# Kernel optimization log

Hardware: AMD Instinct MI355X
Metric: run time of the kernel (lower is better)

## Reference

```python
import jax, jax.numpy as jnp
import numpy as np

N_FFT = 4096
HOP = 1024
WIN = 4096
DIAG_EPS = 1e-7
EPS = 1e-8

# asteroid-style periodic sqrt-hann analysis/synthesis window
_n = np.arange(WIN)
WINDOW = jnp.asarray(np.sqrt(0.5 - 0.5 * np.cos(2.0 * np.pi * _n / WIN)), dtype=jnp.float32)


def _frame_idx(n_samp):
    T = (n_samp - WIN) // HOP + 1
    return np.arange(T)[:, None] * HOP + np.arange(WIN)[None, :]


def stft(x):
    """x: (..., N) -> (real, imag) each (..., F, T) with F = N_FFT//2+1."""
    idx = _frame_idx(x.shape[-1])
    frames = x[..., idx] * WINDOW
    spec = jnp.fft.rfft(frames, axis=-1)     # (..., T, F) complex64
    spec = jnp.moveaxis(spec, -2, -1)        # (..., F, T)
    return spec.real, spec.imag


def istft(re, im, out_len):
    """(..., F, T) -> (..., out_len) via windowed overlap-add."""
    spec = jnp.moveaxis(re + 1j * im, -1, -2)            # (..., T, F)
    frames = jnp.fft.irfft(spec, n=WIN, axis=-1) * WINDOW
    T = frames.shape[-2]
    full = (T - 1) * HOP + WIN
    idx = _frame_idx(full).reshape(-1)
    flat = frames.reshape(frames.shape[:-2] + (-1,))
    out = jnp.zeros(frames.shape[:-2] + (full,), frames.dtype).at[..., idx].add(flat)
    wsq = jnp.zeros((full,), jnp.float32).at[idx].add(jnp.tile(WINDOW ** 2, T))
    out = out / jnp.maximum(wsq, 1e-8)
    return out[..., :out_len]


def psd_causal(re, im):
    """Causal, frame-normalized PSD. re/im: (B, C, F, T) -> complex (B, T, F, C, C)."""
    pr = jnp.einsum('saft,sbft->sabft', re, re) + jnp.einsum('saft,sbft->sabft', im, im)
    pi = jnp.einsum('saft,sbft->sbaft', re, im) - jnp.einsum('saft,sbft->sabft', re, im)
    cnt = jnp.arange(1, re.shape[-1] + 1, dtype=re.dtype)
    pr = jnp.cumsum(pr, -1) / cnt
    pi = jnp.cumsum(pi, -1) / cnt
    psd = pr + 1j * pi                       # (B, a, b, F, T)
    return jnp.transpose(psd, (0, 4, 3, 1, 2))  # (B, T, F, C, C)


def mvdr_vector(psd_s, psd_n):
    """Souden MVDR: ws = inv(Npsd) @ Spsd / (tr(.) + eps). (..., C, C) complex."""
    C = psd_n.shape[-1]
    tr_n = jnp.trace(psd_n, axis1=-2, axis2=-1).real
    epsilon = jax.lax.stop_gradient(tr_n * DIAG_EPS + EPS)
    psd_n = psd_n + epsilon[..., None, None] * jnp.eye(C, dtype=psd_n.dtype)
    num = jnp.linalg.inv(psd_n) @ psd_s
    return num / (jnp.trace(num, axis1=-2, axis2=-1)[..., None, None] + EPS)


def _forward(x, s):
    B, S, C, N = s.shape
    xs = jnp.broadcast_to(x[:, None], (B, S, C, N)).reshape(B * S, C, N)
    ss = s.reshape(B * S, C, N)
    Xr, Xi = stft(xs)
    Sr, Si = stft(ss)
    Nr, Ni = Xr - Sr, Xi - Si
    Sscm = psd_causal(Sr, Si)   # (BS, T, F, C, C)
    Nscm = psd_causal(Nr, Ni)
    ws = mvdr_vector(Sscm, Nscm)  # (BS, T, F, C, C)
    # conj(filter), rearranged to (BS, a, b, F, T)
    fr = jnp.transpose(ws.real, (0, 3, 4, 2, 1))
    fi = -jnp.transpose(ws.imag, (0, 3, 4, 2, 1))
    enh_r = jnp.einsum('sabft,saft->sbft', fr, Xr) - jnp.einsum('sabft,saft->sbft', fi, Xi)
    enh_i = jnp.einsum('sabft,saft->sbft', fr, Xi) + jnp.einsum('sabft,saft->sbft', fi, Xr)
    est = istft(enh_r, enh_i, N)            # (BS, C, N)
    return est.reshape(B, S, C, N)


def setup_inputs() -> dict:
    key = jax.random.key(0)
    kx, ks = jax.random.split(key)
    x = jax.random.normal(kx, (2, 4, 32768), dtype=jnp.float32)
    s = jax.random.normal(ks, (2, 2, 4, 32768), dtype=jnp.float32)
    return {"x": x, "s": s, "do_permute": 0}


def reference(x, s, do_permute):
    # do_permute=False path (PIT permutation is a data-dependent preprocessing step)
    return _forward(x, s)
```

## Files before the change

### kernel.cpp

```cpp
#include <hip/hip_runtime.h>

static constexpr int NFFT = 4096;
static constexpr int HOP  = 1024;
static constexpr int NF   = 2049;
static constexpr int NT   = 29;
static constexpr int NS   = 32768;
static constexpr int NB   = 2;
static constexpr int NSrc = 2;
static constexpr int NC   = 4;
static constexpr int NBS  = NB * NSrc;
static constexpr int FCHUNKS = (NF + 7) / 8;

#define PI_F     3.14159265358979323846f
#define TWO_PI_F 6.28318530717958647692f

#define IDX(a) ((a) + ((a) >> 4))
static constexpr int LDSN = 2048 + 128;

__device__ inline float2 cmul(float2 a, float2 b) {
    return make_float2(a.x * b.x - a.y * b.y, a.x * b.y + a.y * b.x);
}
__device__ inline float2 cmulc(float2 a, float2 b) {
    return make_float2(a.x * b.x + a.y * b.y, a.y * b.x - a.x * b.y);
}

template <int CTRL, int RMASK>
__device__ __forceinline__ float dpp0(float x) {
    return __int_as_float(__builtin_amdgcn_update_dpp(
        0, __float_as_int(x), CTRL, RMASK, 0xF, true));
}

template <int DIR>
__device__ inline void fft4v(float2 v[4]) {
    float2 t0 = make_float2(v[0].x + v[2].x, v[0].y + v[2].y);
    float2 t1 = make_float2(v[0].x - v[2].x, v[0].y - v[2].y);
    float2 t2 = make_float2(v[1].x + v[3].x, v[1].y + v[3].y);
    float2 t3 = make_float2(v[1].x - v[3].x, v[1].y - v[3].y);
    v[0] = make_float2(t0.x + t2.x, t0.y + t2.y);
    v[2] = make_float2(t0.x - t2.x, t0.y - t2.y);
    if (DIR < 0) {
        v[1] = make_float2(t1.x + t3.y, t1.y - t3.x);
        v[3] = make_float2(t1.x - t3.y, t1.y + t3.x);
    } else {
        v[1] = make_float2(t1.x - t3.y, t1.y + t3.x);
        v[3] = make_float2(t1.x + t3.y, t1.y - t3.x);
    }
}

template <int DIR>
__device__ inline void fft8v(float2 v[8]) {
    float2 e[4] = { v[0], v[2], v[4], v[6] };
    float2 o[4] = { v[1], v[3], v[5], v[7] };
    fft4v<DIR>(e);
    fft4v<DIR>(o);
    const float c = 0.70710678118654752f;
    float2 o0 = o[0], o1, o2, o3;
    if (DIR < 0) {
        o1 = make_float2(c * (o[1].x + o[1].y), c * (o[1].y - o[1].x));
        o2 = make_float2(o[2].y, -o[2].x);
        o3 = make_float2(c * (o[3].y - o[3].x), -c * (o[3].x + o[3].y));
    } else {
        o1 = make_float2(c * (o[1].x - o[1].y), c * (o[1].y + o[1].x));
        o2 = make_float2(-o[2].y, o[2].x);
        o3 = make_float2(-c * (o[3].x + o[3].y), c * (o[3].x - o[3].y));
    }
    v[0] = make_float2(e[0].x + o0.x, e[0].y + o0.y);
    v[4] = make_float2(e[0].x - o0.x, e[0].y - o0.y);
    v[1] = make_float2(e[1].x + o1.x, e[1].y + o1.y);
    v[5] = make_float2(e[1].x - o1.x, e[1].y - o1.y);
    v[2] = make_float2(e[2].x + o2.x, e[2].y + o2.y);
    v[6] = make_float2(e[2].x - o2.x, e[2].y - o2.y);
    v[3] = make_float2(e[3].x + o3.x, e[3].y + o3.y);
    v[7] = make_float2(e[3].x - o3.x, e[3].y - o3.y);
}

template <int DIR, int NSs>
__device__ inline void stage8(const float* __restrict__ reS, const float* __restrict__ imS,
                              float* __restrict__ reD, float* __restrict__ imD, int tid) {
    int j = tid;
    float2 v[8];
    #pragma unroll
    for (int r = 0; r < 8; ++r) {
        int a = IDX(j + (r << 8));
        v[r] = make_float2(reS[a], imS[a]);
    }
    if (NSs > 1) {
        float ang = (float)DIR * (TWO_PI_F / (8.0f * (float)NSs)) * (float)(j & (NSs - 1));
        float2 w1; __sincosf(ang, &w1.y, &w1.x);
        float2 w2 = cmul(w1, w1);
        float2 w3 = cmul(w2, w1);
        float2 w4 = cmul(w2, w2);
        float2 w5 = cmul(w3, w2);
        float2 w6 = cmul(w3, w3);
        float2 w7 = cmul(w4, w3);
        v[1] = cmul(v[1], w1);
        v[2] = cmul(v[2], w2);
        v[3] = cmul(v[3], w3);
        v[4] = cmul(v[4], w4);
        v[5] = cmul(v[5], w5);
        v[6] = cmul(v[6], w6);
        v[7] = cmul(v[7], w7);
    }
    fft8v<DIR>(v);
    int idxD = ((j & ~(NSs - 1)) << 3) + (j & (NSs - 1));
    #pragma unroll
    for (int r = 0; r < 8; ++r) {
        int a = IDX(idxD + r * NSs);
        reD[a] = v[r].x;
        imD[a] = v[r].y;
    }
}

template <int DIR>
__device__ inline void stage4_512(const float* __restrict__ reS, const float* __restrict__ imS,
                                  float* __restrict__ reD, float* __restrict__ imD, int tid) {
    #pragma unroll
    for (int h = 0; h < 2; ++h) {
        int j = tid + (h << 8);
        float2 v[4];
        #pragma unroll
        for (int r = 0; r < 4; ++r) {
            int a = IDX(j + (r << 9));
            v[r] = make_float2(reS[a], imS[a]);
        }
        float ang = (float)DIR * (TWO_PI_F / 2048.0f) * (float)j;
        float2 w1; __sincosf(ang, &w1.y, &w1.x);
        float2 w2 = cmul(w1, w1);
        float2 w3 = cmul(w2, w1);
        v[1] = cmul(v[1], w1);
        v[2] = cmul(v[2], w2);
        v[3] = cmul(v[3], w3);
        fft4v<DIR>(v);
        #pragma unroll
        for (int r = 0; r < 4; ++r) {
            int a = IDX(j + (r << 9));
            reD[a] = v[r].x;
            imD[a] = v[r].y;
        }
    }
}

template <int DIR>
__device__ inline void fft2048(float* reA, float* imA, float* reB, float* imB, int tid) {
    stage8<DIR, 1>(reA, imA, reB, imB, tid);  __syncthreads();
    stage8<DIR, 8>(reB, imB, reA, imA, tid);  __syncthreads();
    stage8<DIR, 64>(reA, imA, reB, imB, tid); __syncthreads();
    stage4_512<DIR>(reB, imB, reA, imA, tid); __syncthreads();
}

__global__ __launch_bounds__(256) void stft_kernel(
    const float* __restrict__ x, const float* __restrict__ s,
    float2* __restrict__ Xs, float2* __restrict__ Ss) {
    __shared__ float reA[LDSN], imA[LDSN], reB[LDSN], imB[LDSN];
    int tid = threadIdx.x;
    int fid = blockIdx.x;
    const float* src;
    float2* dst;
    if (fid < NB * NC * NT) {
        int b = fid / (NC * NT);
        int r = fid % (NC * NT);
        int c = r / NT;
        int t = r % NT;
        src = x + (size_t)((b * NC + c) * NS + t * HOP);
        dst = Xs + (size_t)((b * NC + c) * NT + t) * NF;
    } else {
        int g  = fid - NB * NC * NT;
        int bs = g / (NC * NT);
        int r  = g % (NC * NT);
        int c  = r / NT;
        int t  = r % NT;
        src = s + (size_t)((bs * NC + c) * NS + t * HOP);
        dst = Ss + (size_t)((bs * NC + c) * NT + t) * NF;
    }
    const float2* s2 = (const float2*)src;
    for (int n = tid; n < 2048; n += 256) {
        float2 v = s2[n];
        float we = __sinf((float)n * (PI_F / 2048.0f));
        float wo = __sinf((float)(2 * n + 1) * (PI_F / 4096.0f));
        int a = IDX(n);
        reA[a] = v.x * we;
        imA[a] = v.y * wo;
    }
    __syncthreads();
    fft2048<-1>(reA, imA, reB, imB, tid);
    for (int k = tid; k <= 1024; k += 256) {
        int a1 = IDX(k);
        int a2 = IDX((2048 - k) & 2047);
        float2 Za = make_float2(reA[a1], imA[a1]);
        float2 Zb = make_float2(reA[a2], imA[a2]);
        if (k == 0) {
            dst[0]    = make_float2(Za.x + Za.y, 0.f);
            dst[2048] = make_float2(Za.x - Za.y, 0.f);
        } else {
            float2 Ze = make_float2(0.5f * (Za.x + Zb.x),  0.5f * (Za.y - Zb.y));
            float2 Zo = make_float2(0.5f * (Za.y + Zb.y), -0.5f * (Za.x - Zb.x));
            float ang = -(PI_F / 2048.0f) * (float)k;
            float2 W; __sincosf(ang, &W.y, &W.x);
            float2 WZo = cmul(W, Zo);
            dst[k] = make_float2(Ze.x + WZo.x, Ze.y + WZo.y);
            if (k < 1024)
                dst[2048 - k] = make_float2(Ze.x - WZo.x, -(Ze.y - WZo.y));
        }
    }
}

__global__ __launch_bounds__(256, 1) void mvdr2_kernel(
    const float2* __restrict__ Xs, const float2* __restrict__ Ss,
    float2* __restrict__ Es) {
    __shared__ float2 ldsS[4][32][9];
    __shared__ float2 ldsX[4][32][9];
    int tid = threadIdx.x;
    int blk = blockIdx.x;
    int bs  = blk / FCHUNKS;
    int f0  = (blk % FCHUNKS) * 8;
    int b   = bs >> 1;

    for (int idx = tid; idx < 2048; idx += 256) {
        int fi = idx & 7;
        int tt = (idx >> 3) & 31;
        int q  = idx >> 8;
        int c  = q & 3;
        int f  = f0 + fi;
        float2 val = make_float2(0.f, 0.f);
        if (tt < NT && f < NF) {
            val = (q >= 4) ? Xs[(size_t)((b  * NC + c) * NT + tt) * NF + f]
                           : Ss[(size_t)((bs * NC + c) * NT + tt) * NF + f];
        }
        if (q >= 4) ldsX[c][tt][fi] = val; else ldsS[c][tt][fi] = val;
    }
    __syncthreads();

    int lane  = tid & 63;
    int wave  = tid >> 6;
    int t     = lane & 31;
    int fpair = lane >> 5;
    int fi    = wave * 2 + fpair;

    float2 Sv[4], Xv[4], Nv[4];
    #pragma unroll
    for (int c = 0; c < 4; ++c) {
        Sv[c] = ldsS[c][t][fi];
        Xv[c] = ldsX[c][t][fi];
        Nv[c] = make_float2(Xv[c].x - Sv[c].x, Xv[c].y - Sv[c].y);
    }

    float v[32];
    #pragma unroll
    for (int c = 0; c < 4; ++c) {
        v[c]      = Sv[c].x * Sv[c].x + Sv[c].y * Sv[c].y;
        v[16 + c] = Nv[c].x * Nv[c].x + Nv[c].y * Nv[c].y;
    }
    constexpr int PI6[6] = {0, 0, 0, 1, 1, 2};
    constexpr int PJ6[6] = {1, 2, 3, 2, 3, 3};
    #pragma unroll
    for (int p = 0; p < 6; ++p) {
        float2 d = cmulc(Sv[PI6[p]], Sv[PJ6[p]]);
        v[4 + 2 * p] = d.x; v[5 + 2 * p] = d.y;
        d = cmulc(Nv[PI6[p]], Nv[PJ6[p]]);
        v[20 + 2 * p] = d.x; v[21 + 2 * p] = d.y;
    }

    #pragma unroll
    for (int k = 0; k < 32; ++k) v[k] += dpp0<0x111, 0xF>(v[k]);
    #pragma unroll
    for (int k = 0; k < 32; ++k) v[k] += dpp0<0x112, 0xF>(v[k]);
    #pragma unroll
    for (int k = 0; k < 32; ++k) v[k] += dpp0<0x114, 0xF>(v[k]);
    #pragma unroll
    for (int k = 0; k < 32; ++k) v[k] += dpp0<0x118, 0xF>(v[k]);
    #pragma unroll
    for (int k = 0; k < 32; ++k) v[k] += dpp0<0x142, 0xA>(v[k]);

    float pd0 = v[0], pd1 = v[1], pd2 = v[2], pd3 = v[3];
    float2 po0 = make_float2(v[4],  v[5]);
    float2 po1 = make_float2(v[6],  v[7]);
    float2 po2 = make_float2(v[8],  v[9]);
    float2 po3 = make_float2(v[10], v[11]);
    float2 po4 = make_float2(v[12], v[13]);
    float2 po5 = make_float2(v[14], v[15]);
    float eps = (v[16] + v[17] + v[18] + v[19]) * 1e-7f + (float)(t + 1) * 1e-8f;
    float nd0 = v[16] + eps, nd1 = v[17] + eps, nd2 = v[18] + eps, nd3 = v[19] + eps;
    float2 no0 = make_float2(v[20], v[21]);
    float2 no1 = make_float2(v[22], v[23]);
    float2 no2 = make_float2(v[24], v[25]);
    float2 no3 = make_float2(v[26], v[27]);
    float2 no4 = make_float2(v[28], v[29]);
    float2 no5 = make_float2(v[30], v[31]);

    float D0 = nd0;
    float r0 = __builtin_amdgcn_rcpf(D0);
    float2 L10 = make_float2(no0.x * r0, -no0.y * r0);
    float2 L20 = make_float2(no1.x * r0, -no1.y * r0);
    float2 L30 = make_float2(no2.x * r0, -no2.y * r0);
    float D1 = nd1 - (L10.x * L10.x + L10.y * L10.y) * D0;
    float r1 = __builtin_amdgcn_rcpf(D1);
    float2 c10 = make_float2(D0 * L10.x, -D0 * L10.y);
    float2 tA = cmul(L20, c10);
    float2 L21 = make_float2((no3.x - tA.x) * r1, (-no3.y - tA.y) * r1);
    float2 tB = cmul(L30, c10);
    float2 L31 = make_float2((no4.x - tB.x) * r1, (-no4.y - tB.y) * r1);
    float D2 = nd2 - (L20.x * L20.x + L20.y * L20.y) * D0
                   - (L21.x * L21.x + L21.y * L21.y) * D1;
    float r2 = __builtin_amdgcn_rcpf(D2);
    float2 c20 = make_float2(D0 * L20.x, -D0 * L20.y);
    float2 c21 = make_float2(D1 * L21.x, -D1 * L21.y);
    float2 tC = cmul(L30, c20);
    float2 tD = cmul(L31, c21);
    float2 L32 = make_float2((no5.x - tC.x - tD.x) * r2, (-no5.y - tC.y - tD.y) * r2);
    float D3 = nd3 - (L30.x * L30.x + L30.y * L30.y) * D0
                   - (L31.x * L31.x + L31.y * L31.y) * D1
                   - (L32.x * L32.x + L32.y * L32.y) * D2;
    float r3 = __builtin_amdgcn_rcpf(D3);

    float2 u0 = Xv[0];
    float2 m0 = cmul(L10, u0);
    float2 u1 = make_float2(Xv[1].x - m0.x, Xv[1].y - m0.y);
    float2 m1 = cmul(L20, u0), m2 = cmul(L21, u1);
    float2 u2 = make_float2(Xv[2].x - m1.x - m2.x, Xv[2].y - m1.y - m2.y);
    float2 m3 = cmul(L30, u0), m4 = cmul(L31, u1), m5 = cmul(L32, u2);
    float2 u3 = make_float2(Xv[3].x - m3.x - m4.x - m5.x,
                            Xv[3].y - m3.y - m4.y - m5.y);
    float2 w0 = make_float2(u0.x * r0, u0.y * r0);
    float2 w1 = make_float2(u1.x * r1, u1.y * r1);
    float2 w2 = make_float2(u2.x * r2, u2.y * r2);
    float2 w3 = make_float2(u3.x * r3, u3.y * r3);
    float2 z3 = w3;
    float2 n0_ = cmulc(z3, L32);
    float2 z2 = make_float2(w2.x - n0_.x, w2.y - n0_.y);
    float2 n1_ = cmulc(z2, L21), n2_ = cmulc(z3, L31);
    float2 z1 = make_float2(w1.x - n1_.x - n2_.x, w1.y - n1_.y - n2_.y);
    float2 n3_ = cmulc(z1, L10), n4_ = cmulc(z2, L20), n5_ = cmulc(z3, L30);
    float2 z0 = make_float2(w0.x - n3_.x - n4_.x - n5_.x,
                            w0.y - n3_.y - n4_.y - n5_.y);

    float2 K10 = make_float2(-L10.x, -L10.y);
    float2 kk  = cmul(L21, L10);
    float2 K20 = make_float2(kk.x - L20.x, kk.y - L20.y);
    float2 K21 = make_float2(-L21.x, -L21.y);
    kk = cmul(L32, L21);
    float2 K31 = make_float2(kk.x - L31.x, kk.y - L31.y);
    float2 K32 = make_float2(-L32.x, -L32.y);
    float2 ka = cmul(K31, L10), kb = cmul(L32, L20);
    float2 K30 = make_float2(-L30.x - ka.x + kb.x, -L30.y - ka.y + kb.y);

    float q0 = pd0;
    float2 qm = cmul(K10, po0);
    float q1 = pd1 + (K10.x * K10.x + K10.y * K10.y) * pd0 + 2.0f * qm.x;
    qm = cmul(K20, po0);
    float s_a = qm.x * K21.x + qm.y * K21.y;
    qm = cmul(K20, po1);
    float s_b = qm.x;
    qm = cmul(K21, po3);
    float s_c = qm.x;
    float q2 = pd2 + (K20.x * K20.x + K20.y * K20.y) * pd0
                   + (K21.x * K21.x + K21.y * K21.y) * pd1
                   + 2.0f * (s_a + s_b + s_c);
    qm = cmul(K30, po0);
    float s1 = qm.x * K31.x + qm.y * K31.y;
    qm = cmul(K30, po1);
    float s2 = qm.x * K32.x + qm.y * K32.y;
    qm = cmul(K30, po2);
    float s3 = qm.x;
    qm = cmul(K31, po3);
    float s4 = qm.x * K32.x + qm.y * K32.y;
    qm = cmul(K31, po4);
    float s5 = qm.x;
    qm = cmul(K32, po5);
    float s6 = qm.x;
    float q3 = pd3 + (K30.x * K30.x + K30.y * K30.y) * pd0
                   + (K31.x * K31.x + K31.y * K31.y) * pd1
                   + (K32.x * K32.x + K32.y * K32.y) * pd2
                   + 2.0f * (s1 + s2 + s3 + s4 + s5 + s6);
    float tr = q0 * r0 + q1 * r1 + q2 * r2 + q3 * r3;
    float g  = __builtin_amdgcn_rcpf(tr + 1e-8f);

    float2 a0 = cmul(po0, z1), a1 = cmul(po1, z2), a2 = cmul(po2, z3);
    float2 e0 = make_float2(pd0 * z0.x + a0.x + a1.x + a2.x,
                            pd0 * z0.y + a0.y + a1.y + a2.y);
    a0 = cmulc(z0, po0); a1 = cmul(po3, z2); a2 = cmul(po4, z3);
    float2 e1 = make_float2(a0.x + pd1 * z1.x + a1.x + a2.x,
                            a0.y + pd1 * z1.y + a1.y + a2.y);
    a0 = cmulc(z0, po1); a1 = cmulc(z1, po3); a2 = cmul(po5, z3);
    float2 e2 = make_float2(a0.x + a1.x + pd2 * z2.x + a2.x,
                            a0.y + a1.y + pd2 * z2.y + a2.y);
    a0 = cmulc(z0, po2); a1 = cmulc(z1, po4); a2 = cmulc(z2, po5);
    float2 e3 = make_float2(a0.x + a1.x + a2.x + pd3 * z3.x,
                            a0.y + a1.y + a2.y + pd3 * z3.y);
    ldsS[0][t][fi] = make_float2(e0.x * g, e0.y * g);
    ldsS[1][t][fi] = make_float2(e1.x * g, e1.y * g);
    ldsS[2][t][fi] = make_float2(e2.x * g, e2.y * g);
    ldsS[3][t][fi] = make_float2(e3.x * g, e3.y * g);
    __syncthreads();

    for (int idx = tid; idx < 1024; idx += 256) {
        int fi2 = idx & 7;
        int tt  = (idx >> 3) & 31;
        int bo  = idx >> 8;
        int ff  = f0 + fi2;
        if (tt < NT && ff < NF)
            Es[(size_t)((bs * NC + bo) * NT + tt) * NF + ff] = ldsS[bo][tt][fi2];
    }
}

__global__ __launch_bounds__(256) void istft_kernel(
    const float2* __restrict__ Es, float* __restrict__ Fr) {
    __shared__ float reA[LDSN], imA[LDSN], reB[LDSN], imB[LDSN];
    int tid = threadIdx.x;
    int fid = blockIdx.x;
    int bs = fid / (NC * NT);
    int r  = fid % (NC * NT);
    int c  = r / NT;
    int t  = r % NT;
    const float2* src = Es + (size_t)((bs * NC + c) * NT + t) * NF;
    for (int k = tid; k <= 1024; k += 256) {
        float2 A = src[k];
        float2 B = src[2048 - k];
        float2 Ze = make_float2(0.5f * (A.x + B.x), 0.5f * (A.y - B.y));
        float2 D  = make_float2(0.5f * (A.x - B.x), 0.5f * (A.y + B.y));
        float ang = (PI_F / 2048.0f) * (float)k;
        float2 W; __sincosf(ang, &W.y, &W.x);
        float2 Zo = cmul(W, D);
        int a1 = IDX(k);
        reA[a1] = Ze.x - Zo.y;
        imA[a1] = Ze.y + Zo.x;
        if (k > 0 && k < 1024) {
            int a2 = IDX(2048 - k);
            reA[a2] = Ze.x + Zo.y;
            imA[a2] = -Ze.y + Zo.x;
        }
    }
    __syncthreads();
    fft2048<1>(reA, imA, reB, imB, tid);
    float2* d2 = (float2*)(Fr + (size_t)((bs * NC + c) * NT + t) * NFFT);
    for (int n = tid; n < 2048; n += 256) {
        int a = IDX(n);
        float we = __sinf((float)n * (PI_F / 2048.0f)) * (1.0f / 2048.0f);
        float wo = __sinf((float)(2 * n + 1) * (PI_F / 4096.0f)) * (1.0f / 2048.0f);
        d2[n] = make_float2(reA[a] * we, imA[a] * wo);
    }
}

__global__ __launch_bounds__(256) void ola_kernel(
    const float* __restrict__ Fr, float* __restrict__ out) {
    int idx = blockIdx.x * 256 + threadIdx.x;
    const int total = NBS * NC * NS;
    if (idx >= total) return;
    int p  = idx & (NS - 1);
    int ch = idx >> 15;
    int t1 = p >> 10;
    if (t1 > NT - 1) t1 = NT - 1;
    int t0 = (p >= NFFT) ? ((p - (NFFT - 1) + (HOP - 1)) >> 10) : 0;
    float acc = 0.f;
    for (int t = t0; t <= t1; ++t)
        acc += Fr[((size_t)(ch * NT + t) << 12) + (p - (t << 10))];
    float wacc;
    if (t1 - t0 == 3) {
        wacc = 2.0f;
    } else {
        wacc = 0.f;
        for (int t = t0; t <= t1; ++t) {
            float w = __sinf((float)(p - (t << 10)) * (PI_F / 4096.0f));
            wacc += w * w;
        }
    }
    out[idx] = acc / fmaxf(wacc, 1e-8f);
}

extern "C" void kernel_launch(void* const* d_in, const int* in_sizes, int n_in,
                              void* d_out, int out_size, void* d_ws, size_t ws_size,
                              hipStream_t stream) {
    const float* x = (const float*)d_in[0];
    const float* s = (const float*)d_in[1];
    float* out = (float*)d_out;

    const size_t XS_N = (size_t)NB  * NC * NT * NF;
    const size_t SS_N = (size_t)NBS * NC * NT * NF;
    float2* Xs = (float2*)d_ws;
    float2* Ss = Xs + XS_N;
    float2* Es = Ss + SS_N;
    float*  Fr = (float*)(Es + SS_N);

    stft_kernel<<<NB * NC * NT + NBS * NC * NT, 256, 0, stream>>>(x, s, Xs, Ss);

    mvdr2_kernel<<<NBS * FCHUNKS, 256, 0, stream>>>(Xs, Ss, Es);

    istft_kernel<<<NBS * NC * NT, 256, 0, stream>>>(Es, Fr);

    int ola_total = NBS * NC * NS;
    ola_kernel<<<(ola_total + 255) / 256, 256, 0, stream>>>(Fr, out);
}
```

Before: 39.40 us.

## Fuse overlap-add into iSTFT via atomic adds and zero output in STFT

```diff
diff --git a/kernel.cpp b/kernel.cpp
--- a/kernel.cpp
+++ b/kernel.cpp
@@ -150,10 +150,17 @@
 
 __global__ __launch_bounds__(256) void stft_kernel(
     const float* __restrict__ x, const float* __restrict__ s,
-    float2* __restrict__ Xs, float2* __restrict__ Ss) {
+    float2* __restrict__ Xs, float2* __restrict__ Ss,
+    float* __restrict__ out) {
     __shared__ float reA[LDSN], imA[LDSN], reB[LDSN], imB[LDSN];
     int tid = threadIdx.x;
     int fid = blockIdx.x;
+
+    float4* o4 = (float4*)out;
+    const int n4 = (NBS * NC * NS) >> 2;
+    for (int i = fid * 256 + tid; i < n4; i += gridDim.x * 256)
+        o4[i] = make_float4(0.f, 0.f, 0.f, 0.f);
+
     const float* src;
     float2* dst;
     if (fid < NB * NC * NT) {
@@ -402,8 +409,21 @@
     }
 }
 
-__global__ __launch_bounds__(256) void istft_kernel(
-    const float2* __restrict__ Es, float* __restrict__ Fr) {
+__device__ inline float rwsq(int p) {
+    int t1 = p >> 10;
+    if (t1 > NT - 1) t1 = NT - 1;
+    int t0 = (p >= NFFT) ? ((p - (NFFT - 1) + (HOP - 1)) >> 10) : 0;
+    if (t1 - t0 == 3) return 0.5f;
+    float wacc = 0.f;
+    for (int t = t0; t <= t1; ++t) {
+        float w = __sinf((float)(p - (t << 10)) * (PI_F / 4096.0f));
+        wacc += w * w;
+    }
+    return 1.0f / fmaxf(wacc, 1e-8f);
+}
+
+__global__ __launch_bounds__(256) void istft_ola_kernel(
+    const float2* __restrict__ Es, float* __restrict__ out) {
     __shared__ float reA[LDSN], imA[LDSN], reB[LDSN], imB[LDSN];
     int tid = threadIdx.x;
     int fid = blockIdx.x;
@@ -431,39 +451,17 @@
     }
     __syncthreads();
     fft2048<1>(reA, imA, reB, imB, tid);
-    float2* d2 = (float2*)(Fr + (size_t)((bs * NC + c) * NT + t) * NFFT);
+    float* och = out + (size_t)(bs * NC + c) * NS;
+    int base = t * HOP;
     for (int n = tid; n < 2048; n += 256) {
-        int a = IDX(n);
+        int a  = IDX(n);
+        int j0 = 2 * n, j1 = 2 * n + 1;
         float we = __sinf((float)n * (PI_F / 2048.0f)) * (1.0f / 2048.0f);
-        float wo = __sinf((float)(2 * n + 1) * (PI_F / 4096.0f)) * (1.0f / 2048.0f);
-        d2[n] = make_float2(reA[a] * we, imA[a] * wo);
-    }
-}
-
-__global__ __launch_bounds__(256) void ola_kernel(
-    const float* __restrict__ Fr, float* __restrict__ out) {
-    int idx = blockIdx.x * 256 + threadIdx.x;
-    const int total = NBS * NC * NS;
-    if (idx >= total) return;
-    int p  = idx & (NS - 1);
-    int ch = idx >> 15;
-    int t1 = p >> 10;
-    if (t1 > NT - 1) t1 = NT - 1;
-    int t0 = (p >= NFFT) ? ((p - (NFFT - 1) + (HOP - 1)) >> 10) : 0;
-    float acc = 0.f;
-    for (int t = t0; t <= t1; ++t)
-        acc += Fr[((size_t)(ch * NT + t) << 12) + (p - (t << 10))];
-    float wacc;
-    if (t1 - t0 == 3) {
-        wacc = 2.0f;
-    } else {
-        wacc = 0.f;
-        for (int t = t0; t <= t1; ++t) {
-            float w = __sinf((float)(p - (t << 10)) * (PI_F / 4096.0f));
-            wacc += w * w;
-        }
-    }
-    out[idx] = acc / fmaxf(wacc, 1e-8f);
+        float wo = __sinf((float)j1 * (PI_F / 4096.0f)) * (1.0f / 2048.0f);
+        int p0 = base + j0, p1 = base + j1;
+        atomicAdd(&och[p0], reA[a] * we * rwsq(p0));
+        atomicAdd(&och[p1], imA[a] * wo * rwsq(p1));
+    }
 }
 
 extern "C" void kernel_launch(void* const* d_in, const int* in_sizes, int n_in,
@@ -478,14 +476,10 @@
     float2* Xs = (float2*)d_ws;
     float2* Ss = Xs + XS_N;
     float2* Es = Ss + SS_N;
-    float*  Fr = (float*)(Es + SS_N);
-
-    stft_kernel<<<NB * NC * NT + NBS * NC * NT, 256, 0, stream>>>(x, s, Xs, Ss);
+
+    stft_kernel<<<NB * NC * NT + NBS * NC * NT, 256, 0, stream>>>(x, s, Xs, Ss, out);
 
     mvdr2_kernel<<<NBS * FCHUNKS, 256, 0, stream>>>(Xs, Ss, Es);
 
-    istft_kernel<<<NBS * NC * NT, 256, 0, stream>>>(Es, Fr);
-
-    int ola_total = NBS * NC * NS;
-    ola_kernel<<<(ola_total + 255) / 256, 256, 0, stream>>>(Fr, out);
-}
+    istft_ola_kernel<<<NBS * NC * NT, 256, 0, stream>>>(Es, out);
+}
```

Measured after the change: 47.95 us. 1.22x slower.
